# Performance work log

Hardware: AMD Instinct MI355X
Metric: run time of the kernel (lower is better)

## Reference

```python
import jax, jax.numpy as jnp
import numpy as np
from jax import lax

N_CROSS = 2048   # self.n_cross_attention
TOP_K = 256      # hardcoded min(max_k, 256) in forward


def _fps(pts, k):
    """Furthest point sampling. pts: [N,3] -> int32 indices [k]."""
    n = pts.shape[0]

    def body(carry, _):
        dists, last = carry
        d = jnp.sum((pts - pts[last]) ** 2, axis=-1)      # [N]
        dists = jnp.minimum(dists, d)
        nxt = jnp.argmax(dists).astype(jnp.int32)
        return (dists, nxt), last                          # emit index BEFORE update -> first sample is idx 0

    init = (jnp.full((n,), 1e10, dtype=pts.dtype), jnp.int32(0))
    _, idx = lax.scan(body, init, None, length=k)
    return idx


def setup_inputs() -> dict:
    key = jax.random.key(0)
    k1, k2, k3, k4 = jax.random.split(key, 4)
    B, N, C, D = 8, 100000, 18, 128
    return {
        "centerness": jax.random.normal(k1, (B, N), dtype=jnp.float32),
        "cls_scores": jax.random.normal(k2, (B, N, C), dtype=jnp.float32),
        "points": jax.random.normal(k3, (B, N, 3), dtype=jnp.float32) * 3.0,
        "features": jax.random.normal(k4, (B, N, D), dtype=jnp.float32),
    }


def reference(centerness, cls_scores, points, features):
    # select_scores = cls.sigmoid() * centerness.sigmoid().unsqueeze(-1)
    select_scores = jax.nn.sigmoid(cls_scores) * jax.nn.sigmoid(centerness)[..., None]  # [B,N,C]
    max_scores = jnp.max(select_scores, axis=-1)                                         # [B,N]

    # furthest_point_sample(points, n_cross_attention) -> gather features
    cross_inds = jax.vmap(lambda p: _fps(lax.stop_gradient(p), N_CROSS))(points)         # [B,2048]
    cross_features = jnp.take_along_axis(features, cross_inds[..., None], axis=1)        # [B,2048,D]

    # topk(max_scores, 256) then sort indices ascending, gather features/points
    _, inds = lax.top_k(max_scores, TOP_K)                                               # [B,256]
    sort_inds = jnp.sort(inds, axis=-1)                                                  # [B,256]
    feats_sel = jnp.take_along_axis(features, sort_inds[..., None], axis=1)              # [B,256,D]
    pts_sel = jnp.take_along_axis(points, sort_inds[..., None], axis=1)                  # [B,256,3]

    return pts_sel, feats_sel, sort_inds, cross_features
```

## Files before the change

### kernel.cpp

```cpp
#include <hip/hip_runtime.h>
#include <math.h>

#define NB    8
#define NPTS  100000
#define NCLS  18
#define ND    128
#define KFPS  2048
#define KTOP  256

#define FWGS       32
#define FTHR       256
#define FBTHREADS  (FWGS*FTHR)
#define PPT        13
#define NSLOT      32
#define RSTRIDE    64
#define TAG_SHIFT  49
#define KEY_MASK   ((1ull<<TAG_SHIFT)-1)
#define IDX_MASK   0x1FFFFull
#define INVALID_REC (~0ull)

#define BANK_U64   (NSLOT * RSTRIDE)
#define B_TOTAL    (2 * BANK_U64)
#define PART_U64   (NB * B_TOTAL)

static_assert(PPT * FBTHREADS >= NPTS, "coverage");

#define OUT_PTS    0
#define OUT_FEATS  6144
#define OUT_INDS   268288
#define OUT_CROSS  270336
#define OUT_SCORES OUT_CROSS
#define OUT_PART   (OUT_CROSS + 800000)
static_assert((OUT_PART % 2) == 0, "u64 alignment");
static_assert(OUT_PART + PART_U64 * 2 <= OUT_CROSS + 2097152, "fits in region 3");

#define WS_CROSS    16384
#define WS_SORTI    (16384+65536)

__global__ void k_init(unsigned long long* __restrict__ partials) {
  int id = blockIdx.x * 256 + threadIdx.x;
  if (id < PART_U64)
    __hip_atomic_store(&partials[id], INVALID_REC,
                       __ATOMIC_RELAXED, __HIP_MEMORY_SCOPE_AGENT);
}

__global__ void k_scores(const float* __restrict__ cent,
                         const float* __restrict__ cls,
                         float* __restrict__ scores) {
  int gid = blockIdx.x * blockDim.x + threadIdx.x;
  if (gid >= NB * NPTS) return;
  const float* c = cls + (size_t)gid * NCLS;
  float m = c[0];
  #pragma unroll
  for (int i = 1; i < NCLS; ++i) m = fmaxf(m, c[i]);
  double sm = 1.0 / (1.0 + exp(-(double)m));
  double sc = 1.0 / (1.0 + exp(-(double)cent[gid]));
  scores[gid] = __fmul_rn((float)sm, (float)sc);
}

__global__ __launch_bounds__(1024) void k_topk(const float* __restrict__ scores,
                                               int* __restrict__ sorti_ws,
                                               float* __restrict__ out_inds) {
  __shared__ unsigned hist[2048];
  __shared__ int candG[256];
  __shared__ int candE[512];
  __shared__ unsigned s_cg, s_ce, s_bin, s_rank;

  int b = blockIdx.x;
  int tid = threadIdx.x;
  const float* sb = scores + (size_t)b * NPTS;

  unsigned prefix = 0, pmask = 0;
  int r = KTOP;
  for (int pass = 0; pass < 3; ++pass) {
    int shift = (pass == 0) ? 21 : (pass == 1) ? 10 : 0;
    int bins  = (pass < 2) ? 2048 : 1024;
    for (int i = tid; i < bins; i += 1024) hist[i] = 0;
    __syncthreads();
    for (int n = tid; n < NPTS; n += 1024) {
      unsigned k = __float_as_uint(sb[n]);
      if ((k & pmask) == prefix) atomicAdd(&hist[(k >> shift) & (bins - 1)], 1u);
    }
    __syncthreads();
    if (tid == 0) {
      unsigned c = 0; int bin = bins - 1;
      for (; bin > 0; --bin) { unsigned h = hist[bin]; if (c + h >= (unsigned)r) break; c += h; }
      s_bin = (unsigned)bin; s_rank = (unsigned)r - c;
    }
    __syncthreads();
    prefix |= s_bin << shift;
    pmask  |= (unsigned)(bins - 1) << shift;
    r = (int)s_rank;
    __syncthreads();
  }
  unsigned T = prefix;
  int need = r;
  int nG = KTOP - need;

  if (tid == 0) { s_cg = 0; s_ce = 0; }
  __syncthreads();
  for (int n = tid; n < NPTS; n += 1024) {
    unsigned k = __float_as_uint(sb[n]);
    if (k > T)       { unsigned p = atomicAdd(&s_cg, 1u); if (p < 256) candG[p] = n; }
    else if (k == T) { unsigned p = atomicAdd(&s_ce, 1u); if (p < 512) candE[p] = n; }
  }
  __syncthreads();
  unsigned ce = s_ce;
  for (int i = tid; i < 512; i += 1024) if (i >= (int)ce) candE[i] = 0x7FFFFFFF;
  __syncthreads();
  for (int k2 = 2; k2 <= 512; k2 <<= 1)
    for (int j = k2 >> 1; j >= 1; j >>= 1) {
      if (tid < 512) {
        int i = tid, p = i ^ j;
        if (p > i) {
          int a = candE[i], bb = candE[p];
          bool up = ((i & k2) == 0);
          if ((a > bb) == up) { candE[i] = bb; candE[p] = a; }
        }
      }
      __syncthreads();
    }
  int* arr = (int*)hist;
  if (tid < KTOP) arr[tid] = (tid < nG) ? candG[tid] : candE[tid - nG];
  __syncthreads();
  for (int k2 = 2; k2 <= 256; k2 <<= 1)
    for (int j = k2 >> 1; j >= 1; j >>= 1) {
      if (tid < 256) {
        int i = tid, p = i ^ j;
        if (p > i) {
          int a = arr[i], bb = arr[p];
          bool up = ((i & k2) == 0);
          if ((a > bb) == up) { arr[i] = bb; arr[p] = a; }
        }
      }
      __syncthreads();
    }
  if (tid < KTOP) {
    sorti_ws[b * KTOP + tid] = arr[tid];
    out_inds[b * KTOP + tid] = (float)arr[tid];
  }
}

__device__ __forceinline__ void merge2(unsigned long long& b1, unsigned long long& b2,
                                       unsigned long long o1, unsigned long long o2) {
  if (o1 > b1) { unsigned long long t1 = b1; b1 = o1; b2 = (o2 > t1) ? o2 : t1; }
  else         { b2 = (o1 > b2) ? o1 : b2; }
}

__global__ __launch_bounds__(FTHR, 1) void k_fps(const float* __restrict__ points,
                                                 unsigned long long* __restrict__ partials,
                                                 int* __restrict__ cross_inds) {
  int b    = blockIdx.x & 7;
  int wg   = blockIdx.x >> 3;
  int tid  = threadIdx.x;
  int lane = tid & 63;
  int wave = tid >> 6;
  int gthr = wg * FTHR + tid;

  __shared__ unsigned long long lred[4][2];
  __shared__ unsigned long long lg[2];

  const float* pb = points + (size_t)b * NPTS * 3;
  unsigned long long* base = partials + (size_t)b * B_TOTAL;

  float px[PPT], py[PPT], pz[PPT], dd[PPT];
  #pragma unroll
  for (int i = 0; i < PPT; ++i) {
    int n = gthr + i * FBTHREADS;
    bool v = (n < NPTS);
    px[i] = v ? pb[3 * n + 0] : 0.f;
    py[i] = v ? pb[3 * n + 1] : 0.f;
    pz[i] = v ? pb[3 * n + 2] : 0.f;
    dd[i] = 1e10f;
  }
  if (wg == 0 && tid == 0) cross_inds[b * KFPS] = 0;

  int w = 0;
  int t = 1;
  int c = 0;
  while (t < KFPS) {
    float wx = pb[3 * w + 0];
    float wy = pb[3 * w + 1];
    float wz = pb[3 * w + 2];

    unsigned long long b1 = 0ull, b2 = 0ull;
    #pragma unroll
    for (int i = 0; i < PPT; ++i) {
      int n = gthr + i * FBTHREADS;
      float dx = __fsub_rn(px[i], wx);
      float dy = __fsub_rn(py[i], wy);
      float dz = __fsub_rn(pz[i], wz);
      float s  = __fadd_rn(__fadd_rn(__fmul_rn(dx, dx), __fmul_rn(dy, dy)), __fmul_rn(dz, dz));
      float nd = fminf(dd[i], s);
      dd[i] = nd;
      if (n < NPTS) {
        unsigned long long k = ((unsigned long long)__float_as_uint(nd) << 17) |
                               (unsigned long long)(0x1FFFFu ^ (unsigned)n);
        if (k > b1) { b2 = b1; b1 = k; } else if (k > b2) { b2 = k; }
      }
    }
    #pragma unroll
    for (int off = 32; off >= 1; off >>= 1) {
      unsigned long long o1 = __shfl_xor(b1, off);
      unsigned long long o2 = __shfl_xor(b2, off);
      merge2(b1, b2, o1, o2);
    }
    if (lane == 0) { lred[wave][0] = b1; lred[wave][1] = b2; }
    __syncthreads();

    unsigned tag = (unsigned)c + 1u;
    unsigned long long* bank = base + (size_t)(c & 1) * BANK_U64;
    if (wave == 0) {
      unsigned long long rec1 = 0, rec2 = 0;
      if (lane == 0) {
        unsigned long long m1 = lred[0][0], m2 = lred[0][1];
        merge2(m1, m2, lred[1][0], lred[1][1]);
        merge2(m1, m2, lred[2][0], lred[2][1]);
        merge2(m1, m2, lred[3][0], lred[3][1]);
        rec1 = ((unsigned long long)tag << TAG_SHIFT) | m1;
        rec2 = ((unsigned long long)tag << TAG_SHIFT) | m2;
        __hip_atomic_store(&bank[(size_t)wg * RSTRIDE + 0], rec1,
                           __ATOMIC_RELAXED, __HIP_MEMORY_SCOPE_AGENT);
        __hip_atomic_store(&bank[(size_t)wg * RSTRIDE + 1], rec2,
                           __ATOMIC_RELAXED, __HIP_MEMORY_SCOPE_AGENT);
      }
      unsigned long long r1 = 0, r2 = 0;
      unsigned long long* a0 = &bank[(size_t)(lane & 31) * RSTRIDE + 0];
      unsigned long long* a1 = &bank[(size_t)(lane & 31) * RSTRIDE + 1];
      int spins = 0;
      for (;;) {
        if (lane < 32) {
          r1 = __hip_atomic_load(a0, __ATOMIC_RELAXED, __HIP_MEMORY_SCOPE_AGENT);
          r2 = __hip_atomic_load(a1, __ATOMIC_RELAXED, __HIP_MEMORY_SCOPE_AGENT);
        }
        bool ok = (lane >= 32) || (((unsigned)(r1 >> TAG_SHIFT) == tag) &&
                                   ((unsigned)(r2 >> TAG_SHIFT) == tag));
        if (__all((int)ok)) break;
        ++spins;
        if (spins > (1 << 11)) break;
        if ((spins & 255) == 0 && lane == 0) {
          __hip_atomic_store(&bank[(size_t)wg * RSTRIDE + 0], rec1,
                             __ATOMIC_RELAXED, __HIP_MEMORY_SCOPE_AGENT);
          __hip_atomic_store(&bank[(size_t)wg * RSTRIDE + 1], rec2,
                             __ATOMIC_RELAXED, __HIP_MEMORY_SCOPE_AGENT);
        }
        if (spins > 512) __builtin_amdgcn_s_sleep(1);
      }
      unsigned long long k1 = (lane < 32) ? (r1 & KEY_MASK) : 0ull;
      unsigned long long k2 = (lane < 32) ? (r2 & KEY_MASK) : 0ull;
      #pragma unroll
      for (int off = 32; off >= 1; off >>= 1) {
        unsigned long long o1 = __shfl_xor(k1, off);
        unsigned long long o2 = __shfl_xor(k2, off);
        merge2(k1, k2, o1, o2);
      }
      if (lane == 0) { lg[0] = k1; lg[1] = k2; }
    }
    __syncthreads();
    unsigned long long g1 = lg[0], g2 = lg[1];
    ++c;

    int idx1 = (int)(0x1FFFFu ^ (unsigned)(g1 & IDX_MASK));
    int idx2 = (int)(0x1FFFFu ^ (unsigned)(g2 & IDX_MASK));
    if (idx1 >= NPTS) idx1 = 0;
    if (idx2 >= NPTS) idx2 = 0;
    float v2f = __uint_as_float((unsigned)(g2 >> 17));

    if (wg == 0 && tid == 0) cross_inds[b * KFPS + t] = idx1;
    ++t;
    if (t >= KFPS) break;

    float w1x = pb[3 * idx1 + 0], w1y = pb[3 * idx1 + 1], w1z = pb[3 * idx1 + 2];
    float p2x = pb[3 * idx2 + 0], p2y = pb[3 * idx2 + 1], p2z = pb[3 * idx2 + 2];
    float sx = __fsub_rn(p2x, w1x);
    float sy = __fsub_rn(p2y, w1y);
    float sz = __fsub_rn(p2z, w1z);
    float d2 = __fadd_rn(__fadd_rn(__fmul_rn(sx, sx), __fmul_rn(sy, sy)), __fmul_rn(sz, sz));
    bool spec = (v2f > 0.f) && (d2 >= v2f) && (idx2 != idx1);

    if (spec) {
      #pragma unroll
      for (int i = 0; i < PPT; ++i) {
        float dx = __fsub_rn(px[i], w1x);
        float dy = __fsub_rn(py[i], w1y);
        float dz = __fsub_rn(pz[i], w1z);
        float s  = __fadd_rn(__fadd_rn(__fmul_rn(dx, dx), __fmul_rn(dy, dy)), __fmul_rn(dz, dz));
        dd[i] = fminf(dd[i], s);
      }
      if (wg == 0 && tid == 0) cross_inds[b * KFPS + t] = idx2;
      ++t;
      w = idx2;
    } else {
      w = idx1;
    }
  }
}

#define GF4 ((NB * (KTOP + KFPS)) * (ND / 4))
#define GPTS (NB * KTOP * 3)

__global__ void k_gather(const float* __restrict__ pts,
                         const float* __restrict__ feat,
                         const int* __restrict__ sorti,
                         const int* __restrict__ crossi,
                         float* __restrict__ out) {
  int id = blockIdx.x * 256 + threadIdx.x;
  if (id < GF4) {
    int row = id >> 5, c4 = id & 31;
    int b, s; float* dst;
    if (row < NB * KTOP) {
      b = row >> 8;
      s = sorti[row];
      dst = out + OUT_FEATS + (size_t)row * ND;
    } else {
      int r2 = row - NB * KTOP;
      b = r2 >> 11;
      s = crossi[r2];
      dst = out + OUT_CROSS + (size_t)r2 * ND;
    }
    if (s < 0 || s >= NPTS) s = 0;
    float4 v = ((const float4*)(feat + ((size_t)b * NPTS + (size_t)s) * ND))[c4];
    ((float4*)dst)[c4] = v;
  } else if (id < GF4 + GPTS) {
    int q = id - GF4;
    int row = q / 3, d = q - row * 3;
    int b = row >> 8;
    int s = sorti[row];
    if (s < 0 || s >= NPTS) s = 0;
    out[OUT_PTS + q] = pts[((size_t)b * NPTS + (size_t)s) * 3 + d];
  }
}

extern "C" void kernel_launch(void* const* d_in, const int* in_sizes, int n_in,
                              void* d_out, int out_size, void* d_ws, size_t ws_size,
                              hipStream_t stream) {
  const float* cent = (const float*)d_in[0];
  const float* cls  = (const float*)d_in[1];
  const float* pts  = (const float*)d_in[2];
  const float* feat = (const float*)d_in[3];
  float* out = (float*)d_out;

  unsigned long long* partials = (unsigned long long*)(out + OUT_PART);
  int* cross_ws = (int*)((char*)d_ws + WS_CROSS);
  int* sorti_ws = (int*)((char*)d_ws + WS_SORTI);
  float* scores = out + OUT_SCORES;

  hipLaunchKernelGGL(k_init, dim3((PART_U64 + 255) / 256), dim3(256), 0, stream,
                     partials);
  hipLaunchKernelGGL(k_scores, dim3((NB * NPTS + 255) / 256), dim3(256), 0, stream,
                     cent, cls, scores);
  hipLaunchKernelGGL(k_topk, dim3(NB), dim3(1024), 0, stream,
                     scores, sorti_ws, out + OUT_INDS);
  hipLaunchKernelGGL(k_fps, dim3(NB * FWGS), dim3(FTHR), 0, stream,
                     pts, partials, cross_ws);
  int gtot = GF4 + GPTS;
  hipLaunchKernelGGL(k_gather, dim3((gtot + 255) / 256), dim3(256), 0, stream,
                     pts, feat, sorti_ws, cross_ws, out);
}
```

Baseline: 3.960 ms.

## Extend FPS speculation from top-2 to top-4 candidates per global reduction

The FPS kernel now reduces the top-4 distance keys per round instead of top-2, across lanes, waves and workgroups. It then accepts up to three extra samples speculatively when each candidate stays at least as far from the newly chosen points as its own current distance. The aim is to cut the number of cross-workgroup barrier rounds, which dominate the serial 2048-step loop. In exchange, each round does more shuffles, compare-exchange work and atomic loads and stores, and the speculation only pays off when candidates stay valid.

```diff
diff --git a/kernel.cpp b/kernel.cpp
--- a/kernel.cpp
+++ b/kernel.cpp
@@ -141,10 +141,21 @@
   }
 }
 
-__device__ __forceinline__ void merge2(unsigned long long& b1, unsigned long long& b2,
-                                       unsigned long long o1, unsigned long long o2) {
-  if (o1 > b1) { unsigned long long t1 = b1; b1 = o1; b2 = (o2 > t1) ? o2 : t1; }
-  else         { b2 = (o1 > b2) ? o1 : b2; }
+__device__ __forceinline__ void ce_u64(unsigned long long& x, unsigned long long& y) {
+  unsigned long long mx = (x > y) ? x : y;
+  unsigned long long mn = (x > y) ? y : x;
+  x = mx; y = mn;
+}
+__device__ __forceinline__ void merge4(unsigned long long& a1, unsigned long long& a2,
+                                       unsigned long long& a3, unsigned long long& a4,
+                                       unsigned long long b1, unsigned long long b2,
+                                       unsigned long long b3, unsigned long long b4) {
+  unsigned long long t1 = (a1 > b4) ? a1 : b4;
+  unsigned long long t2 = (a2 > b3) ? a2 : b3;
+  unsigned long long t3 = (a3 > b2) ? a3 : b2;
+  unsigned long long t4 = (a4 > b1) ? a4 : b1;
+  ce_u64(t1, t3); ce_u64(t2, t4); ce_u64(t1, t2); ce_u64(t3, t4);
+  a1 = t1; a2 = t2; a3 = t3; a4 = t4;
 }
 
 __global__ __launch_bounds__(FTHR, 1) void k_fps(const float* __restrict__ points,
@@ -157,8 +168,8 @@
   int wave = tid >> 6;
   int gthr = wg * FTHR + tid;
 
-  __shared__ unsigned long long lred[4][2];
-  __shared__ unsigned long long lg[2];
+  __shared__ unsigned long long lred[4][4];
+  __shared__ unsigned long long lg[4];
 
   const float* pb = points + (size_t)b * NPTS * 3;
   unsigned long long* base = partials + (size_t)b * B_TOTAL;
@@ -175,6 +186,18 @@
   }
   if (wg == 0 && tid == 0) cross_inds[b * KFPS] = 0;
 
+  #define FOLD(fx, fy, fz) do {                                               \
+    _Pragma("unroll")                                                         \
+    for (int i_ = 0; i_ < PPT; ++i_) {                                        \
+      float dx_ = __fsub_rn(px[i_], (fx));                                    \
+      float dy_ = __fsub_rn(py[i_], (fy));                                    \
+      float dz_ = __fsub_rn(pz[i_], (fz));                                    \
+      float s_  = __fadd_rn(__fadd_rn(__fmul_rn(dx_, dx_), __fmul_rn(dy_, dy_)), \
+                            __fmul_rn(dz_, dz_));                             \
+      dd[i_] = fminf(dd[i_], s_);                                             \
+    }                                                                         \
+  } while (0)
+
   int w = 0;
   int t = 1;
   int c = 0;
@@ -183,7 +206,7 @@
     float wy = pb[3 * w + 1];
     float wz = pb[3 * w + 2];
 
-    unsigned long long b1 = 0ull, b2 = 0ull;
+    unsigned long long s1 = 0ull, s2 = 0ull, s3 = 0ull, s4 = 0ull;
     #pragma unroll
     for (int i = 0; i < PPT; ++i) {
       int n = gthr + i * FBTHREADS;
@@ -196,104 +219,144 @@
       if (n < NPTS) {
         unsigned long long k = ((unsigned long long)__float_as_uint(nd) << 17) |
                                (unsigned long long)(0x1FFFFu ^ (unsigned)n);
-        if (k > b1) { b2 = b1; b1 = k; } else if (k > b2) { b2 = k; }
+        s4 = (k > s4) ? k : s4;
+        ce_u64(s3, s4); ce_u64(s2, s3); ce_u64(s1, s2);
       }
     }
     #pragma unroll
     for (int off = 32; off >= 1; off >>= 1) {
-      unsigned long long o1 = __shfl_xor(b1, off);
-      unsigned long long o2 = __shfl_xor(b2, off);
-      merge2(b1, b2, o1, o2);
-    }
-    if (lane == 0) { lred[wave][0] = b1; lred[wave][1] = b2; }
+      unsigned long long o1 = __shfl_xor(s1, off);
+      unsigned long long o2 = __shfl_xor(s2, off);
+      unsigned long long o3 = __shfl_xor(s3, off);
+      unsigned long long o4 = __shfl_xor(s4, off);
+      merge4(s1, s2, s3, s4, o1, o2, o3, o4);
+    }
+    if (lane == 0) { lred[wave][0] = s1; lred[wave][1] = s2;
+                     lred[wave][2] = s3; lred[wave][3] = s4; }
     __syncthreads();
 
     unsigned tag = (unsigned)c + 1u;
     unsigned long long* bank = base + (size_t)(c & 1) * BANK_U64;
     if (wave == 0) {
-      unsigned long long rec1 = 0, rec2 = 0;
+      unsigned long long rc[4] = {0, 0, 0, 0};
       if (lane == 0) {
-        unsigned long long m1 = lred[0][0], m2 = lred[0][1];
-        merge2(m1, m2, lred[1][0], lred[1][1]);
-        merge2(m1, m2, lred[2][0], lred[2][1]);
-        merge2(m1, m2, lred[3][0], lred[3][1]);
-        rec1 = ((unsigned long long)tag << TAG_SHIFT) | m1;
-        rec2 = ((unsigned long long)tag << TAG_SHIFT) | m2;
-        __hip_atomic_store(&bank[(size_t)wg * RSTRIDE + 0], rec1,
-                           __ATOMIC_RELAXED, __HIP_MEMORY_SCOPE_AGENT);
-        __hip_atomic_store(&bank[(size_t)wg * RSTRIDE + 1], rec2,
-                           __ATOMIC_RELAXED, __HIP_MEMORY_SCOPE_AGENT);
-      }
-      unsigned long long r1 = 0, r2 = 0;
-      unsigned long long* a0 = &bank[(size_t)(lane & 31) * RSTRIDE + 0];
-      unsigned long long* a1 = &bank[(size_t)(lane & 31) * RSTRIDE + 1];
+        unsigned long long m1 = lred[0][0], m2 = lred[0][1],
+                           m3 = lred[0][2], m4 = lred[0][3];
+        merge4(m1, m2, m3, m4, lred[1][0], lred[1][1], lred[1][2], lred[1][3]);
+        merge4(m1, m2, m3, m4, lred[2][0], lred[2][1], lred[2][2], lred[2][3]);
+        merge4(m1, m2, m3, m4, lred[3][0], lred[3][1], lred[3][2], lred[3][3]);
+        rc[0] = ((unsigned long long)tag << TAG_SHIFT) | m1;
+        rc[1] = ((unsigned long long)tag << TAG_SHIFT) | m2;
+        rc[2] = ((unsigned long long)tag << TAG_SHIFT) | m3;
+        rc[3] = ((unsigned long long)tag << TAG_SHIFT) | m4;
+        #pragma unroll
+        for (int q = 0; q < 4; ++q)
+          __hip_atomic_store(&bank[(size_t)wg * RSTRIDE + q], rc[q],
+                             __ATOMIC_RELAXED, __HIP_MEMORY_SCOPE_AGENT);
+      }
+      unsigned long long r1 = 0, r2 = 0, r3 = 0, r4 = 0;
+      unsigned long long* a0 = &bank[(size_t)(lane & 31) * RSTRIDE];
       int spins = 0;
       for (;;) {
         if (lane < 32) {
-          r1 = __hip_atomic_load(a0, __ATOMIC_RELAXED, __HIP_MEMORY_SCOPE_AGENT);
-          r2 = __hip_atomic_load(a1, __ATOMIC_RELAXED, __HIP_MEMORY_SCOPE_AGENT);
+          r1 = __hip_atomic_load(a0 + 0, __ATOMIC_RELAXED, __HIP_MEMORY_SCOPE_AGENT);
+          r2 = __hip_atomic_load(a0 + 1, __ATOMIC_RELAXED, __HIP_MEMORY_SCOPE_AGENT);
+          r3 = __hip_atomic_load(a0 + 2, __ATOMIC_RELAXED, __HIP_MEMORY_SCOPE_AGENT);
+          r4 = __hip_atomic_load(a0 + 3, __ATOMIC_RELAXED, __HIP_MEMORY_SCOPE_AGENT);
         }
-        bool ok = (lane >= 32) || (((unsigned)(r1 >> TAG_SHIFT) == tag) &&
-                                   ((unsigned)(r2 >> TAG_SHIFT) == tag));
+        bool ok = (lane >= 32) ||
+                  (((unsigned)(r1 >> TAG_SHIFT) == tag) &&
+                   ((unsigned)(r2 >> TAG_SHIFT) == tag) &&
+                   ((unsigned)(r3 >> TAG_SHIFT) == tag) &&
+                   ((unsigned)(r4 >> TAG_SHIFT) == tag));
         if (__all((int)ok)) break;
         ++spins;
         if (spins > (1 << 11)) break;
         if ((spins & 255) == 0 && lane == 0) {
-          __hip_atomic_store(&bank[(size_t)wg * RSTRIDE + 0], rec1,
-                             __ATOMIC_RELAXED, __HIP_MEMORY_SCOPE_AGENT);
-          __hip_atomic_store(&bank[(size_t)wg * RSTRIDE + 1], rec2,
-                             __ATOMIC_RELAXED, __HIP_MEMORY_SCOPE_AGENT);
+          #pragma unroll
+          for (int q = 0; q < 4; ++q)
+            __hip_atomic_store(&bank[(size_t)wg * RSTRIDE + q], rc[q],
+                               __ATOMIC_RELAXED, __HIP_MEMORY_SCOPE_AGENT);
         }
         if (spins > 512) __builtin_amdgcn_s_sleep(1);
       }
       unsigned long long k1 = (lane < 32) ? (r1 & KEY_MASK) : 0ull;
       unsigned long long k2 = (lane < 32) ? (r2 & KEY_MASK) : 0ull;
+      unsigned long long k3 = (lane < 32) ? (r3 & KEY_MASK) : 0ull;
+      unsigned long long k4 = (lane < 32) ? (r4 & KEY_MASK) : 0ull;
       #pragma unroll
       for (int off = 32; off >= 1; off >>= 1) {
         unsigned long long o1 = __shfl_xor(k1, off);
         unsigned long long o2 = __shfl_xor(k2, off);
-        merge2(k1, k2, o1, o2);
-      }
-      if (lane == 0) { lg[0] = k1; lg[1] = k2; }
-    }
-    __syncthreads();
-    unsigned long long g1 = lg[0], g2 = lg[1];
+        unsigned long long o3 = __shfl_xor(k3, off);
+        unsigned long long o4 = __shfl_xor(k4, off);
+        merge4(k1, k2, k3, k4, o1, o2, o3, o4);
+      }
+      if (lane == 0) { lg[0] = k1; lg[1] = k2; lg[2] = k3; lg[3] = k4; }
+    }
+    __syncthreads();
+    unsigned long long g1 = lg[0], g2 = lg[1], g3 = lg[2], g4 = lg[3];
     ++c;
 
-    int idx1 = (int)(0x1FFFFu ^ (unsigned)(g1 & IDX_MASK));
-    int idx2 = (int)(0x1FFFFu ^ (unsigned)(g2 & IDX_MASK));
-    if (idx1 >= NPTS) idx1 = 0;
-    if (idx2 >= NPTS) idx2 = 0;
-    float v2f = __uint_as_float((unsigned)(g2 >> 17));
-
-    if (wg == 0 && tid == 0) cross_inds[b * KFPS + t] = idx1;
-    ++t;
+    int i1 = (int)(0x1FFFFu ^ (unsigned)(g1 & IDX_MASK));
+    int i2 = (int)(0x1FFFFu ^ (unsigned)(g2 & IDX_MASK));
+    int i3 = (int)(0x1FFFFu ^ (unsigned)(g3 & IDX_MASK));
+    int i4 = (int)(0x1FFFFu ^ (unsigned)(g4 & IDX_MASK));
+    if (i1 >= NPTS) i1 = 0;
+    if (i2 >= NPTS) i2 = 0;
+    if (i3 >= NPTS) i3 = 0;
+    if (i4 >= NPTS) i4 = 0;
+    float v2 = __uint_as_float((unsigned)(g2 >> 17));
+    float v3 = __uint_as_float((unsigned)(g3 >> 17));
+    float v4 = __uint_as_float((unsigned)(g4 >> 17));
+
+    if (wg == 0 && tid == 0) cross_inds[b * KFPS + t] = i1;
+    ++t; w = i1;
     if (t >= KFPS) break;
 
-    float w1x = pb[3 * idx1 + 0], w1y = pb[3 * idx1 + 1], w1z = pb[3 * idx1 + 2];
-    float p2x = pb[3 * idx2 + 0], p2y = pb[3 * idx2 + 1], p2z = pb[3 * idx2 + 2];
-    float sx = __fsub_rn(p2x, w1x);
-    float sy = __fsub_rn(p2y, w1y);
-    float sz = __fsub_rn(p2z, w1z);
-    float d2 = __fadd_rn(__fadd_rn(__fmul_rn(sx, sx), __fmul_rn(sy, sy)), __fmul_rn(sz, sz));
-    bool spec = (v2f > 0.f) && (d2 >= v2f) && (idx2 != idx1);
-
-    if (spec) {
-      #pragma unroll
-      for (int i = 0; i < PPT; ++i) {
-        float dx = __fsub_rn(px[i], w1x);
-        float dy = __fsub_rn(py[i], w1y);
-        float dz = __fsub_rn(pz[i], w1z);
-        float s  = __fadd_rn(__fadd_rn(__fmul_rn(dx, dx), __fmul_rn(dy, dy)), __fmul_rn(dz, dz));
-        dd[i] = fminf(dd[i], s);
-      }
-      if (wg == 0 && tid == 0) cross_inds[b * KFPS + t] = idx2;
-      ++t;
-      w = idx2;
-    } else {
-      w = idx1;
-    }
-  }
+    float e0x = pb[3 * i1 + 0], e0y = pb[3 * i1 + 1], e0z = pb[3 * i1 + 2];
+
+    {
+      float cx = pb[3 * i2 + 0], cy = pb[3 * i2 + 1], cz = pb[3 * i2 + 2];
+      float dx = __fsub_rn(cx, e0x), dy = __fsub_rn(cy, e0y), dz = __fsub_rn(cz, e0z);
+      float d2 = __fadd_rn(__fadd_rn(__fmul_rn(dx, dx), __fmul_rn(dy, dy)), __fmul_rn(dz, dz));
+      if (!((v2 > 0.f) && (d2 >= v2) && (i2 != i1))) continue;
+      FOLD(e0x, e0y, e0z);
+      if (wg == 0 && tid == 0) cross_inds[b * KFPS + t] = i2;
+      ++t; w = i2;
+      if (t >= KFPS) break;
+    }
+    float e1x = pb[3 * i2 + 0], e1y = pb[3 * i2 + 1], e1z = pb[3 * i2 + 2];
+
+    {
+      float cx = pb[3 * i3 + 0], cy = pb[3 * i3 + 1], cz = pb[3 * i3 + 2];
+      float ax = __fsub_rn(cx, e0x), ay = __fsub_rn(cy, e0y), az = __fsub_rn(cz, e0z);
+      float da = __fadd_rn(__fadd_rn(__fmul_rn(ax, ax), __fmul_rn(ay, ay)), __fmul_rn(az, az));
+      float bx = __fsub_rn(cx, e1x), by = __fsub_rn(cy, e1y), bz = __fsub_rn(cz, e1z);
+      float db = __fadd_rn(__fadd_rn(__fmul_rn(bx, bx), __fmul_rn(by, by)), __fmul_rn(bz, bz));
+      if (!((v3 > 0.f) && (da >= v3) && (db >= v3))) continue;
+      FOLD(e1x, e1y, e1z);
+      if (wg == 0 && tid == 0) cross_inds[b * KFPS + t] = i3;
+      ++t; w = i3;
+      if (t >= KFPS) break;
+    }
+    float e2x = pb[3 * i3 + 0], e2y = pb[3 * i3 + 1], e2z = pb[3 * i3 + 2];
+
+    {
+      float cx = pb[3 * i4 + 0], cy = pb[3 * i4 + 1], cz = pb[3 * i4 + 2];
+      float ax = __fsub_rn(cx, e0x), ay = __fsub_rn(cy, e0y), az = __fsub_rn(cz, e0z);
+      float da = __fadd_rn(__fadd_rn(__fmul_rn(ax, ax), __fmul_rn(ay, ay)), __fmul_rn(az, az));
+      float bx = __fsub_rn(cx, e1x), by = __fsub_rn(cy, e1y), bz = __fsub_rn(cz, e1z);
+      float db = __fadd_rn(__fadd_rn(__fmul_rn(bx, bx), __fmul_rn(by, by)), __fmul_rn(bz, bz));
+      float gx = __fsub_rn(cx, e2x), gy = __fsub_rn(cy, e2y), gz = __fsub_rn(cz, e2z);
+      float dg = __fadd_rn(__fadd_rn(__fmul_rn(gx, gx), __fmul_rn(gy, gy)), __fmul_rn(gz, gz));
+      if (!((v4 > 0.f) && (da >= v4) && (db >= v4) && (dg >= v4))) continue;
+      FOLD(e2x, e2y, e2z);
+      if (wg == 0 && tid == 0) cross_inds[b * KFPS + t] = i4;
+      ++t; w = i4;
+    }
+  }
+  #undef FOLD
 }
 
 #define GF4 ((NB * (KTOP + KFPS)) * (ND / 4))
```

New measurement: 4.300 ms. 8.6% more time.
